# Optimization experiments

Hardware: AMD Instinct MI355X
Metric: run time of the kernel (lower is better)

Reference implementation:

```python
import jax, jax.numpy as jnp
import numpy as np

B, F, O = 32, 26, 20
IN, G = 2048, 512
REL = 53
EPS = 1e-5  # BatchNorm1d default eps


def setup_inputs() -> dict:
    key = jax.random.key(0)
    ks = jax.random.split(key, 10)
    inp = {
        "region_feats": jax.random.normal(ks[0], (B, F, O, IN), jnp.float32),
        "region_masks": jnp.ones((B, F, O), jnp.float32),
        "rel_feats": jax.random.randint(ks[1], (B, F, O, O), 0, REL, jnp.int64),
        "tem_feats": jax.random.uniform(ks[2], (B, F * O, F * O), jnp.float32),
        # learned params (eval mode: dropout off, BN uses running stats)
        "rel_W": jax.random.normal(ks[3], (G, IN), jnp.float32) * (1.0 / np.sqrt(IN)),
        "rel_b": jnp.zeros((G,), jnp.float32),
        "rel_emb": jax.random.normal(ks[4], (REL, G), jnp.float32) * 0.02,
        "tem_W": jax.random.normal(ks[5], (G, IN), jnp.float32) * (1.0 / np.sqrt(IN)),
        "tem_b": jnp.zeros((G,), jnp.float32),
        "bn_w": jnp.ones((F * O,), jnp.float32),
        "bn_b": jnp.zeros((F * O,), jnp.float32),
        "bn_rm": jnp.zeros((F * O,), jnp.float32),
        "bn_rv": jnp.ones((F * O,), jnp.float32),
    }
    return inp


def reference(region_feats, region_masks, rel_feats, tem_feats,
              rel_W, rel_b, rel_emb, tem_W, tem_b,
              bn_w, bn_b, bn_rm, bn_rv):
    b, f, o, _ = region_feats.shape
    # ---- RELATIONAL FEATURE GRAPH ----
    # [B,F,O,G]
    rel_region = jnp.einsum("bfoi,gi->bfog", region_feats, rel_W) + rel_b
    # embedding lookup: [B,F,O,O,G]
    emb = rel_emb[rel_feats]
    mask = (rel_feats > 0).astype(region_feats.dtype)  # [B,F,O,O]
    msum = jnp.sum(mask, axis=3)                        # [B,F,O]
    # sum_j mask_ij * emb_ij  (masked reduction over neighbor dim)
    emb_sum = jnp.einsum("bfijg,bfij->bfig", emb, mask)
    # sum_j mask_ij * r_i == r_i * msum_i, so (emb_sum + r*msum)/msum
    rel_out = (emb_sum + rel_region * msum[..., None]) / msum[..., None]
    rel_out = rel_out.reshape(b, f * o, -1)
    # ---- TEMPORAL FEATURE GRAPH ----
    tem_region = jnp.einsum("bfoi,gi->bfog", region_feats, tem_W) + tem_b
    tem_region = tem_region.reshape(b, f * o, -1)
    tem_sum = jnp.sum(tem_feats, axis=2)                # [B, F*O]
    tem_out = jnp.matmul(tem_feats, tem_region) / tem_sum[..., None]
    # ---- OUTPUT ----
    out = jnp.concatenate([rel_out, tem_out], axis=-1)  # [B, F*O, 2G]
    out = jnp.tanh(out)
    # BatchNorm1d over channel dim 1 (eval mode, running stats)
    inv = bn_w / jnp.sqrt(bn_rv + EPS)                  # [F*O]
    out = (out - bn_rm[None, :, None]) * inv[None, :, None] + bn_b[None, :, None]
    return out
```

## Files before the change

kernel.cpp:

```cpp
#include <hip/hip_runtime.h>
#include <stdint.h>

#define BB 32
#define FO 520
#define M1 16640
#define KIN 2048
#define KA 2112
#define N1 1024
#define GG 512
#define K2P 576
#define M2 640

typedef unsigned short u16;
typedef short v8s __attribute__((ext_vector_type(8)));
typedef float v4f __attribute__((ext_vector_type(4)));

__device__ __forceinline__ u16 f2bf(float f) {
  union { float f; unsigned u; } v; v.f = f;
  unsigned r = v.u + 0x7fffu + ((v.u >> 16) & 1u);
  return (u16)(r >> 16);
}

__device__ __forceinline__ float fast_tanh(float x) {
  float cx = fminf(fmaxf(x, -15.f), 15.f);
  float e = __expf(2.f * cx);
  return (e - 1.f) / (e + 1.f);
}

__global__ void prep_all_kernel(const float* __restrict__ rf, const int* __restrict__ rel,
                                const float* __restrict__ relW, const float* __restrict__ temW,
                                const float* __restrict__ emb, const float* __restrict__ tem,
                                u16* __restrict__ A1, u16* __restrict__ Wc,
                                u16* __restrict__ A2, float* __restrict__ tsum) {
  const int blk = blockIdx.x;
  const int t = threadIdx.x;
  if (blk < M1 + 1024) {
    const float* src;
    u16* orow;
    if (blk < M1) { src = rf + (size_t)blk * KIN; orow = A1 + (size_t)blk * KA; }
    else {
      const int n = blk - M1;
      src = (n < GG) ? (relW + (size_t)n * KIN) : (temW + (size_t)(n - GG) * KIN);
      orow = Wc + (size_t)n * KA;
    }
    const float4* p = (const float4*)src;
    float4 a = p[2 * t], b = p[2 * t + 1];
    v8s v;
    v[0] = (short)f2bf(a.x); v[1] = (short)f2bf(a.y);
    v[2] = (short)f2bf(a.z); v[3] = (short)f2bf(a.w);
    v[4] = (short)f2bf(b.x); v[5] = (short)f2bf(b.y);
    v[6] = (short)f2bf(b.z); v[7] = (short)f2bf(b.w);
    *(v8s*)(orow + t * 8) = v;
    if (t < 64) {
      float sval = 0.f;
      if (blk < M1) {
        const int* rp = rel + (size_t)blk * 20;
        int cnt = 0, ms = 0;
#pragma unroll
        for (int j = 0; j < 20; ++j) { int ix = rp[j]; cnt += (ix == t + 1); ms += (ix > 0); }
        if (t < 52 && ms > 0) sval = (float)cnt / (float)ms;
      } else {
        const int n = blk - M1;
        if (n < GG && t < 52) sval = emb[(size_t)(t + 1) * GG + n];
      }
      orow[KIN + t] = f2bf(sval);
    }
    return;
  }
  const int w = t >> 6, l = t & 63;
  const int row = (blk - (M1 + 1024)) * 4 + w;
  const int b = row / M2, i = row % M2;
  u16* orow = A2 + (size_t)row * K2P;
  v8s z = {0, 0, 0, 0, 0, 0, 0, 0};
  if (i >= FO) {
    *(v8s*)(orow + l * 8) = z;
    if (l < 8) *(v8s*)(orow + (64 + l) * 8) = z;
    return;
  }
  const float* srow = tem + ((size_t)b * FO + i) * FO;
  float s = 0.f;
  {
    float4 a = *(const float4*)(srow + 8 * l);
    float4 bb = *(const float4*)(srow + 8 * l + 4);
    s += a.x + a.y + a.z + a.w + bb.x + bb.y + bb.z + bb.w;
    v8s v;
    v[0] = (short)f2bf(a.x); v[1] = (short)f2bf(a.y);
    v[2] = (short)f2bf(a.z); v[3] = (short)f2bf(a.w);
    v[4] = (short)f2bf(bb.x); v[5] = (short)f2bf(bb.y);
    v[6] = (short)f2bf(bb.z); v[7] = (short)f2bf(bb.w);
    *(v8s*)(orow + l * 8) = v;
  }
  if (l < 8) {
    if (l == 0) {
      float4 a = *(const float4*)(srow + 512);
      float4 bb = *(const float4*)(srow + 516);
      s += a.x + a.y + a.z + a.w + bb.x + bb.y + bb.z + bb.w;
      v8s v;
      v[0] = (short)f2bf(a.x); v[1] = (short)f2bf(a.y);
      v[2] = (short)f2bf(a.z); v[3] = (short)f2bf(a.w);
      v[4] = (short)f2bf(bb.x); v[5] = (short)f2bf(bb.y);
      v[6] = (short)f2bf(bb.z); v[7] = (short)f2bf(bb.w);
      *(v8s*)(orow + 512) = v;
    } else {
      *(v8s*)(orow + (64 + l) * 8) = z;
    }
  }
#pragma unroll
  for (int off = 32; off > 0; off >>= 1) s += __shfl_down(s, off);
  if (l == 0) tsum[(size_t)b * FO + i] = s;
}

__global__ __launch_bounds__(256) void gemm1_kernel(
    const u16* __restrict__ A, const u16* __restrict__ Wc,
    const float* __restrict__ rel_b, const float* __restrict__ tem_b,
    const float* __restrict__ bn_w, const float* __restrict__ bn_b,
    const float* __restrict__ bn_rm, const float* __restrict__ bn_rv,
    float* __restrict__ out, u16* __restrict__ BT) {
  __shared__ u16 smem[8704];
  u16* As = smem;
  u16* Bs = smem + 4096;
  const int tid = threadIdx.x;
  const int lane = tid & 63;
  const int wv = tid >> 6, wm = wv >> 1, wn = wv & 1;
  const int id = blockIdx.x;
  const int x = id & 7, s = id >> 3;
  int mt, ntile;
  if (s < 128) { mt = x * 16 + (s >> 3); ntile = s & 7; }
  else         { mt = 128 + (s - 128);   ntile = x; }
  const int m0 = mt * 128, n0 = ntile * 128;
  const int quad = lane >> 4, r16 = lane & 15;

  const u16* ga[2]; const u16* gb[2];
  u16* la[2]; u16* lb[2];
#pragma unroll
  for (int i = 0; i < 2; ++i) {
    const int L = i * 256 + tid;
    const int r = L >> 2, sl = L & 3;
    const int c = sl ^ ((r >> 1) & 3);
    ga[i] = A + (size_t)(m0 + r) * KA + c * 8;
    gb[i] = Wc + (size_t)(n0 + r) * KA + c * 8;
    la[i] = &As[(size_t)(i * 256 + wv * 64) * 8];
    lb[i] = &Bs[(size_t)(i * 256 + wv * 64) * 8];
  }

  v4f acc[4][4];
#pragma unroll
  for (int i = 0; i < 4; ++i)
#pragma unroll
    for (int j = 0; j < 4; ++j) { v4f z = {0.f, 0.f, 0.f, 0.f}; acc[i][j] = z; }

  for (int k0 = 0; k0 < KA; k0 += 32) {
    __syncthreads();
#pragma unroll
    for (int i = 0; i < 2; ++i) {
      __builtin_amdgcn_global_load_lds((const __attribute__((address_space(1))) void*)ga[i],
                                       (__attribute__((address_space(3))) void*)la[i], 16, 0, 0);
      __builtin_amdgcn_global_load_lds((const __attribute__((address_space(1))) void*)gb[i],
                                       (__attribute__((address_space(3))) void*)lb[i], 16, 0, 0);
      ga[i] += 32; gb[i] += 32;
    }
    __syncthreads();
    v8s af[4], bf[4];
#pragma unroll
    for (int t4 = 0; t4 < 4; ++t4) {
      const int ra = wm * 64 + t4 * 16 + r16;
      const int rb = wn * 64 + t4 * 16 + r16;
      af[t4] = *(const v8s*)&As[ra * 32 + ((quad ^ ((ra >> 1) & 3)) * 8)];
      bf[t4] = *(const v8s*)&Bs[rb * 32 + ((quad ^ ((rb >> 1) & 3)) * 8)];
    }
#pragma unroll
    for (int mtt = 0; mtt < 4; ++mtt)
#pragma unroll
      for (int ntt = 0; ntt < 4; ++ntt)
        acc[mtt][ntt] = __builtin_amdgcn_mfma_f32_16x16x32_bf16(af[mtt], bf[ntt], acc[mtt][ntt], 0, 0, 0);
  }

  if (n0 < GG) {
#pragma unroll
    for (int mtt = 0; mtt < 4; ++mtt) {
      const int mb = m0 + wm * 64 + mtt * 16 + quad * 4;
      const int bb = mb / FO;
      const int fo0 = mb - bb * FO;
      float inv[4], rm[4], bofs[4];
#pragma unroll
      for (int r = 0; r < 4; ++r) {
        const int fo = fo0 + r;
        inv[r] = bn_w[fo] * rsqrtf(bn_rv[fo] + 1e-5f);
        rm[r] = bn_rm[fo]; bofs[r] = bn_b[fo];
      }
#pragma unroll
      for (int ntt = 0; ntt < 4; ++ntt) {
        const int n = n0 + wn * 64 + ntt * 16 + r16;
        const float rbn = rel_b[n];
#pragma unroll
        for (int r = 0; r < 4; ++r) {
          float val = (fast_tanh(acc[mtt][ntt][r] + rbn) - rm[r]) * inv[r] + bofs[r];
          __builtin_nontemporal_store(val, out + (size_t)(mb + r) * N1 + n);
        }
      }
    }
  } else {
    __syncthreads();
#pragma unroll
    for (int p = 0; p < 2; ++p) {
      if (p) __syncthreads();
      if (wn == p) {
#pragma unroll
        for (int mtt = 0; mtt < 4; ++mtt) {
          const int il = wm * 64 + mtt * 16 + quad * 4;
#pragma unroll
          for (int ntt = 0; ntt < 4; ++ntt) {
            const int gl = ntt * 16 + r16;
            const float tb = tem_b[(n0 - GG) + p * 64 + gl];
            ushort4 w;
            w.x = f2bf(acc[mtt][ntt][0] + tb);
            w.y = f2bf(acc[mtt][ntt][1] + tb);
            w.z = f2bf(acc[mtt][ntt][2] + tb);
            w.w = f2bf(acc[mtt][ntt][3] + tb);
            *(ushort4*)&smem[gl * 136 + il] = w;
          }
        }
      }
      __syncthreads();
#pragma unroll
      for (int pass = 0; pass < 4; ++pass) {
        const int gl = pass * 16 + (tid >> 4);
        const int ch = tid & 15;
        const int m = m0 + ch * 8;
        const int b1 = m / FO;
        const int i1 = m - b1 * FO;
        v8s val = *(const v8s*)&smem[gl * 136 + ch * 8];
        const int g = (n0 - GG) + p * 64 + gl;
        *(v8s*)(BT + ((size_t)(b1 * GG + g)) * K2P + i1) = val;
      }
    }
  }
}

__global__ __launch_bounds__(256) void gemm2_kernel(
    const u16* __restrict__ A2, const u16* __restrict__ BT,
    const float* __restrict__ tsum,
    const float* __restrict__ bn_w, const float* __restrict__ bn_b,
    const float* __restrict__ bn_rm, const float* __restrict__ bn_rv,
    float* __restrict__ out) {
  __shared__ u16 smem[2 * 64 * 64];
  u16* As = smem;
  u16* Bs = smem + 4096;
  const int tid = threadIdx.x;
  const int lane = tid & 63;
  const int wv = tid >> 6, wm = wv >> 1, wn = wv & 1;
  const int m0 = blockIdx.x * 64;
  const int n0 = blockIdx.y * 64;
  const int b = blockIdx.z;
  const u16* Ab = A2 + (size_t)b * M2 * K2P;
  const u16* Bb = BT + (size_t)b * GG * K2P;
  const int quad = lane >> 4, r16 = lane & 15;

  const u16* gp[4]; u16* lp[4];
#pragma unroll
  for (int i = 0; i < 4; ++i) {
    const int L = i * 256 + tid;
    const int tile = L >> 9;
    const int idx = L & 511;
    const int r = idx >> 3, sl = idx & 7;
    const int c = sl ^ (r & 7);
    gp[i] = (tile ? (Bb + (size_t)(n0 + r) * K2P) : (Ab + (size_t)(m0 + r) * K2P)) + c * 8;
    lp[i] = (tile ? Bs : As) + (size_t)((i & 1) * 256 + wv * 64) * 8;
  }

  v4f acc[2][2];
#pragma unroll
  for (int i = 0; i < 2; ++i)
#pragma unroll
    for (int j = 0; j < 2; ++j) { v4f z = {0.f, 0.f, 0.f, 0.f}; acc[i][j] = z; }

  for (int k0 = 0; k0 < K2P; k0 += 64) {
    __syncthreads();
#pragma unroll
    for (int i = 0; i < 4; ++i) {
      __builtin_amdgcn_global_load_lds((const __attribute__((address_space(1))) void*)gp[i],
                                       (__attribute__((address_space(3))) void*)lp[i], 16, 0, 0);
      gp[i] += 64;
    }
    __syncthreads();
#pragma unroll
    for (int ks = 0; ks < 2; ++ks) {
      v8s af[2], bf[2];
#pragma unroll
      for (int t4 = 0; t4 < 2; ++t4) {
        const int ra = wm * 32 + t4 * 16 + r16;
        const int rb = wn * 32 + t4 * 16 + r16;
        af[t4] = *(const v8s*)&As[ra * 64 + (((ks * 4 + quad) ^ (ra & 7)) * 8)];
        bf[t4] = *(const v8s*)&Bs[rb * 64 + (((ks * 4 + quad) ^ (rb & 7)) * 8)];
      }
#pragma unroll
      for (int mtt = 0; mtt < 2; ++mtt)
#pragma unroll
        for (int ntt = 0; ntt < 2; ++ntt)
          acc[mtt][ntt] = __builtin_amdgcn_mfma_f32_16x16x32_bf16(af[mtt], bf[ntt], acc[mtt][ntt], 0, 0, 0);
    }
  }

#pragma unroll
  for (int mtt = 0; mtt < 2; ++mtt) {
    const int ibase = m0 + wm * 32 + mtt * 16 + quad * 4;
    float ts[4], inv[4], rm[4], bofs[4];
#pragma unroll
    for (int r = 0; r < 4; ++r) {
      const int i = ibase + r;
      if (i < FO) {
        ts[r] = 1.f / tsum[(size_t)b * FO + i];
        inv[r] = bn_w[i] * rsqrtf(bn_rv[i] + 1e-5f);
        rm[r] = bn_rm[i]; bofs[r] = bn_b[i];
      }
    }
#pragma unroll
    for (int ntt = 0; ntt < 2; ++ntt) {
      const int g = n0 + wn * 32 + ntt * 16 + r16;
#pragma unroll
      for (int r = 0; r < 4; ++r) {
        const int i = ibase + r;
        if (i < FO) {
          float val = (fast_tanh(acc[mtt][ntt][r] * ts[r]) - rm[r]) * inv[r] + bofs[r];
          __builtin_nontemporal_store(val, out + ((size_t)(b * FO + i)) * N1 + GG + g);
        }
      }
    }
  }
}

extern "C" void kernel_launch(void* const* d_in, const int* in_sizes, int n_in,
                              void* d_out, int out_size, void* d_ws, size_t ws_size,
                              hipStream_t stream) {
  const float* region_feats = (const float*)d_in[0];
  const int* rel_feats = (const int*)d_in[2];
  const float* tem_feats = (const float*)d_in[3];
  const float* rel_W = (const float*)d_in[4];
  const float* rel_b = (const float*)d_in[5];
  const float* rel_emb = (const float*)d_in[6];
  const float* tem_W = (const float*)d_in[7];
  const float* tem_b = (const float*)d_in[8];
  const float* bn_w = (const float*)d_in[9];
  const float* bn_b = (const float*)d_in[10];
  const float* bn_rm = (const float*)d_in[11];
  const float* bn_rv = (const float*)d_in[12];
  float* out = (float*)d_out;

  char* base = (char*)d_ws;
  u16* A1 = (u16*)base;
  u16* Wc = (u16*)(base + 70287360);
  u16* A2 = (u16*)(base + 74612736);
  u16* BT = (u16*)(base + 98205696);
  float* tsum = (float*)(base + 117080064);

  prep_all_kernel<<<M1 + 1024 + 5120, 256, 0, stream>>>(
      region_feats, rel_feats, rel_W, tem_W, rel_emb, tem_feats, A1, Wc, A2, tsum);
  gemm1_kernel<<<1040, 256, 0, stream>>>(A1, Wc, rel_b, tem_b,
                                         bn_w, bn_b, bn_rm, bn_rv, out, BT);
  gemm2_kernel<<<dim3(10, 8, 32), 256, 0, stream>>>(A2, BT, tsum,
                                                    bn_w, bn_b, bn_rm, bn_rv, out);
}
```

Measured before the change: 438.2 us.

## Double-buffer LDS tiles in both GEMM kernels to overlap loads with MFMA

Both GEMM kernels now use two LDS stages. The next K-slice is issued with global_load_lds into the alternate buffer while MFMAs run on the current one, which cuts one barrier per iteration and hides global-load latency behind compute. LDS use grows to 32KB per block, which may lower occupancy. Correctness depends on the single trailing __syncthreads also waiting for the async LDS loads (vmcnt) to finish before the buffers swap.

```diff
diff --git a/kernel.cpp b/kernel.cpp
--- a/kernel.cpp
+++ b/kernel.cpp
@@ -116,9 +116,7 @@
     const float* __restrict__ bn_w, const float* __restrict__ bn_b,
     const float* __restrict__ bn_rm, const float* __restrict__ bn_rv,
     float* __restrict__ out, u16* __restrict__ BT) {
-  __shared__ u16 smem[8704];
-  u16* As = smem;
-  u16* Bs = smem + 4096;
+  __shared__ u16 smem[16384];
   const int tid = threadIdx.x;
   const int lane = tid & 63;
   const int wv = tid >> 6, wm = wv >> 1, wn = wv & 1;
@@ -131,7 +129,7 @@
   const int quad = lane >> 4, r16 = lane & 15;
 
   const u16* ga[2]; const u16* gb[2];
-  u16* la[2]; u16* lb[2];
+  int lofA[2], lofB[2];
 #pragma unroll
   for (int i = 0; i < 2; ++i) {
     const int L = i * 256 + tid;
@@ -139,8 +137,8 @@
     const int c = sl ^ ((r >> 1) & 3);
     ga[i] = A + (size_t)(m0 + r) * KA + c * 8;
     gb[i] = Wc + (size_t)(n0 + r) * KA + c * 8;
-    la[i] = &As[(size_t)(i * 256 + wv * 64) * 8];
-    lb[i] = &Bs[(size_t)(i * 256 + wv * 64) * 8];
+    lofA[i] = (i * 256 + wv * 64) * 8;
+    lofB[i] = 4096 + (i * 256 + wv * 64) * 8;
   }
 
   v4f acc[4][4];
@@ -149,17 +147,31 @@
 #pragma unroll
     for (int j = 0; j < 4; ++j) { v4f z = {0.f, 0.f, 0.f, 0.f}; acc[i][j] = z; }
 
+#pragma unroll
+  for (int i = 0; i < 2; ++i) {
+    __builtin_amdgcn_global_load_lds((const __attribute__((address_space(1))) void*)ga[i],
+                                     (__attribute__((address_space(3))) void*)(smem + lofA[i]), 16, 0, 0);
+    __builtin_amdgcn_global_load_lds((const __attribute__((address_space(1))) void*)gb[i],
+                                     (__attribute__((address_space(3))) void*)(smem + lofB[i]), 16, 0, 0);
+    ga[i] += 32; gb[i] += 32;
+  }
+  __syncthreads();
+
+  int cur = 0;
   for (int k0 = 0; k0 < KA; k0 += 32) {
-    __syncthreads();
-#pragma unroll
-    for (int i = 0; i < 2; ++i) {
-      __builtin_amdgcn_global_load_lds((const __attribute__((address_space(1))) void*)ga[i],
-                                       (__attribute__((address_space(3))) void*)la[i], 16, 0, 0);
-      __builtin_amdgcn_global_load_lds((const __attribute__((address_space(1))) void*)gb[i],
-                                       (__attribute__((address_space(3))) void*)lb[i], 16, 0, 0);
-      ga[i] += 32; gb[i] += 32;
-    }
-    __syncthreads();
+    if (k0 + 32 < KA) {
+      u16* dst = smem + (cur ^ 1) * 8192;
+#pragma unroll
+      for (int i = 0; i < 2; ++i) {
+        __builtin_amdgcn_global_load_lds((const __attribute__((address_space(1))) void*)ga[i],
+                                         (__attribute__((address_space(3))) void*)(dst + lofA[i]), 16, 0, 0);
+        __builtin_amdgcn_global_load_lds((const __attribute__((address_space(1))) void*)gb[i],
+                                         (__attribute__((address_space(3))) void*)(dst + lofB[i]), 16, 0, 0);
+        ga[i] += 32; gb[i] += 32;
+      }
+    }
+    const u16* As = smem + cur * 8192;
+    const u16* Bs = As + 4096;
     v8s af[4], bf[4];
 #pragma unroll
     for (int t4 = 0; t4 < 4; ++t4) {
@@ -173,6 +185,8 @@
 #pragma unroll
       for (int ntt = 0; ntt < 4; ++ntt)
         acc[mtt][ntt] = __builtin_amdgcn_mfma_f32_16x16x32_bf16(af[mtt], bf[ntt], acc[mtt][ntt], 0, 0, 0);
+    __syncthreads();
+    cur ^= 1;
   }
 
   if (n0 < GG) {
@@ -243,9 +257,7 @@
     const float* __restrict__ bn_w, const float* __restrict__ bn_b,
     const float* __restrict__ bn_rm, const float* __restrict__ bn_rv,
     float* __restrict__ out) {
-  __shared__ u16 smem[2 * 64 * 64];
-  u16* As = smem;
-  u16* Bs = smem + 4096;
+  __shared__ u16 smem[16384];
   const int tid = threadIdx.x;
   const int lane = tid & 63;
   const int wv = tid >> 6, wm = wv >> 1, wn = wv & 1;
@@ -256,7 +268,7 @@
   const u16* Bb = BT + (size_t)b * GG * K2P;
   const int quad = lane >> 4, r16 = lane & 15;
 
-  const u16* gp[4]; u16* lp[4];
+  const u16* gp[4]; int lof[4];
 #pragma unroll
   for (int i = 0; i < 4; ++i) {
     const int L = i * 256 + tid;
@@ -265,7 +277,7 @@
     const int r = idx >> 3, sl = idx & 7;
     const int c = sl ^ (r & 7);
     gp[i] = (tile ? (Bb + (size_t)(n0 + r) * K2P) : (Ab + (size_t)(m0 + r) * K2P)) + c * 8;
-    lp[i] = (tile ? Bs : As) + (size_t)((i & 1) * 256 + wv * 64) * 8;
+    lof[i] = (tile ? 4096 : 0) + ((i & 1) * 256 + wv * 64) * 8;
   }
 
   v4f acc[2][2];
@@ -274,15 +286,27 @@
 #pragma unroll
     for (int j = 0; j < 2; ++j) { v4f z = {0.f, 0.f, 0.f, 0.f}; acc[i][j] = z; }
 
+#pragma unroll
+  for (int i = 0; i < 4; ++i) {
+    __builtin_amdgcn_global_load_lds((const __attribute__((address_space(1))) void*)gp[i],
+                                     (__attribute__((address_space(3))) void*)(smem + lof[i]), 16, 0, 0);
+    gp[i] += 64;
+  }
+  __syncthreads();
+
+  int cur = 0;
   for (int k0 = 0; k0 < K2P; k0 += 64) {
-    __syncthreads();
-#pragma unroll
-    for (int i = 0; i < 4; ++i) {
-      __builtin_amdgcn_global_load_lds((const __attribute__((address_space(1))) void*)gp[i],
-                                       (__attribute__((address_space(3))) void*)lp[i], 16, 0, 0);
-      gp[i] += 64;
-    }
-    __syncthreads();
+    if (k0 + 64 < K2P) {
+      u16* dst = smem + (cur ^ 1) * 8192;
+#pragma unroll
+      for (int i = 0; i < 4; ++i) {
+        __builtin_amdgcn_global_load_lds((const __attribute__((address_space(1))) void*)gp[i],
+                                         (__attribute__((address_space(3))) void*)(dst + lof[i]), 16, 0, 0);
+        gp[i] += 64;
+      }
+    }
+    const u16* As = smem + cur * 8192;
+    const u16* Bs = As + 4096;
 #pragma unroll
     for (int ks = 0; ks < 2; ++ks) {
       v8s af[2], bf[2];
@@ -299,6 +323,8 @@
         for (int ntt = 0; ntt < 2; ++ntt)
           acc[mtt][ntt] = __builtin_amdgcn_mfma_f32_16x16x32_bf16(af[mtt], bf[ntt], acc[mtt][ntt], 0, 0, 0);
     }
+    __syncthreads();
+    cur ^= 1;
   }
 
 #pragma unroll
```

Result: no change. 431.0 us (-1.6%).

## Triple-buffer LDS pipeline in both GEMMs and enlarge gemm2 tiles

Applied to the files above, without the earlier changes.

Both GEMM kernels replace the single-buffered load-then-compute loop with a three-stage LDS ring. Global-to-LDS loads for K-step t+2 are issued while step t is computed, synchronised with explicit vmcnt waits and s_barrier. The aim is to hide global memory latency behind MFMA work instead of stalling on two __syncthreads per K-step. gemm2 also moves from 64x64 to 128x128 tiles with a 4x4 MFMA fragment per wave, which cuts the block count and increases operand reuse. The cost is more LDS per block (48 KB), which lowers occupancy, and hand-written waitcnt sequencing that must match the number of loads in flight exactly.

```diff
diff --git a/kernel.cpp b/kernel.cpp
--- a/kernel.cpp
+++ b/kernel.cpp
@@ -110,15 +110,57 @@
   if (l == 0) tsum[(size_t)b * FO + i] = s;
 }
 
+
+#define STAGE4(DST)                                                                              \
+  do {                                                                                           \
+    u16* dst_ = smem + (DST);                                                                    \
+    __builtin_amdgcn_global_load_lds((const __attribute__((address_space(1))) void*)ga0,         \
+        (__attribute__((address_space(3))) void*)(dst_ + lofA0), 16, 0, 0);                      \
+    __builtin_amdgcn_global_load_lds((const __attribute__((address_space(1))) void*)gb0,         \
+        (__attribute__((address_space(3))) void*)(dst_ + lofB0), 16, 0, 0);                      \
+    __builtin_amdgcn_global_load_lds((const __attribute__((address_space(1))) void*)ga1,         \
+        (__attribute__((address_space(3))) void*)(dst_ + lofA1), 16, 0, 0);                      \
+    __builtin_amdgcn_global_load_lds((const __attribute__((address_space(1))) void*)gb1,         \
+        (__attribute__((address_space(3))) void*)(dst_ + lofB1), 16, 0, 0);                      \
+    ga0 += 32; gb0 += 32; ga1 += 32; gb1 += 32;                                                  \
+  } while (0)
+
+#define COMPUTE16(CB)                                                                            \
+  do {                                                                                           \
+    const u16* As_ = smem + (CB) * 8192;                                                         \
+    const u16* Bs_ = As_ + 4096;                                                                 \
+    v8s af[4], bf[4];                                                                            \
+    _Pragma("unroll") for (int t4 = 0; t4 < 4; ++t4) {                                           \
+      const int ra = wm * 64 + t4 * 16 + r16;                                                    \
+      const int rb = wn * 64 + t4 * 16 + r16;                                                    \
+      af[t4] = *(const v8s*)&As_[ra * 32 + ((quad ^ ((ra >> 1) & 3)) * 8)];                      \
+      bf[t4] = *(const v8s*)&Bs_[rb * 32 + ((quad ^ ((rb >> 1) & 3)) * 8)];                      \
+    }                                                                                            \
+    _Pragma("unroll") for (int mtt = 0; mtt < 4; ++mtt)                                          \
+      _Pragma("unroll") for (int ntt = 0; ntt < 4; ++ntt)                                        \
+        acc[mtt][ntt] =                                                                          \
+            __builtin_amdgcn_mfma_f32_16x16x32_bf16(af[mtt], bf[ntt], acc[mtt][ntt], 0, 0, 0);   \
+  } while (0)
+
+#define PIPE_TAIL(CB0, CB1)                                                                      \
+  do {                                                                                           \
+    asm volatile("s_waitcnt vmcnt(4)" ::: "memory");                                             \
+    __builtin_amdgcn_s_barrier();                                                                \
+    COMPUTE16(CB0);                                                                              \
+    asm volatile("s_waitcnt lgkmcnt(0)" ::: "memory");                                           \
+    __builtin_amdgcn_s_barrier();                                                                \
+    asm volatile("s_waitcnt vmcnt(0)" ::: "memory");                                             \
+    __builtin_amdgcn_s_barrier();                                                                \
+    COMPUTE16(CB1);                                                                              \
+  } while (0)
+
 __global__ __launch_bounds__(256) void gemm1_kernel(
     const u16* __restrict__ A, const u16* __restrict__ Wc,
     const float* __restrict__ rel_b, const float* __restrict__ tem_b,
     const float* __restrict__ bn_w, const float* __restrict__ bn_b,
     const float* __restrict__ bn_rm, const float* __restrict__ bn_rv,
     float* __restrict__ out, u16* __restrict__ BT) {
-  __shared__ u16 smem[8704];
-  u16* As = smem;
-  u16* Bs = smem + 4096;
+  __shared__ u16 smem[24576];
   const int tid = threadIdx.x;
   const int lane = tid & 63;
   const int wv = tid >> 6, wm = wv >> 1, wn = wv & 1;
@@ -130,18 +172,20 @@
   const int m0 = mt * 128, n0 = ntile * 128;
   const int quad = lane >> 4, r16 = lane & 15;
 
-  const u16* ga[2]; const u16* gb[2];
-  u16* la[2]; u16* lb[2];
-#pragma unroll
-  for (int i = 0; i < 2; ++i) {
-    const int L = i * 256 + tid;
-    const int r = L >> 2, sl = L & 3;
-    const int c = sl ^ ((r >> 1) & 3);
-    ga[i] = A + (size_t)(m0 + r) * KA + c * 8;
-    gb[i] = Wc + (size_t)(n0 + r) * KA + c * 8;
-    la[i] = &As[(size_t)(i * 256 + wv * 64) * 8];
-    lb[i] = &Bs[(size_t)(i * 256 + wv * 64) * 8];
-  }
+  const u16 *ga0, *ga1, *gb0, *gb1;
+  {
+    const int r0 = tid >> 2, sl0 = tid & 3;
+    const int c0 = sl0 ^ ((r0 >> 1) & 3);
+    ga0 = A + (size_t)(m0 + r0) * KA + c0 * 8;
+    gb0 = Wc + (size_t)(n0 + r0) * KA + c0 * 8;
+    const int L1 = 256 + tid;
+    const int r1 = L1 >> 2, sl1 = L1 & 3;
+    const int c1 = sl1 ^ ((r1 >> 1) & 3);
+    ga1 = A + (size_t)(m0 + r1) * KA + c1 * 8;
+    gb1 = Wc + (size_t)(n0 + r1) * KA + c1 * 8;
+  }
+  const int lofA0 = wv * 512, lofA1 = 2048 + wv * 512;
+  const int lofB0 = 4096 + wv * 512, lofB1 = 6144 + wv * 512;
 
   v4f acc[4][4];
 #pragma unroll
@@ -149,31 +193,21 @@
 #pragma unroll
     for (int j = 0; j < 4; ++j) { v4f z = {0.f, 0.f, 0.f, 0.f}; acc[i][j] = z; }
 
-  for (int k0 = 0; k0 < KA; k0 += 32) {
-    __syncthreads();
-#pragma unroll
-    for (int i = 0; i < 2; ++i) {
-      __builtin_amdgcn_global_load_lds((const __attribute__((address_space(1))) void*)ga[i],
-                                       (__attribute__((address_space(3))) void*)la[i], 16, 0, 0);
-      __builtin_amdgcn_global_load_lds((const __attribute__((address_space(1))) void*)gb[i],
-                                       (__attribute__((address_space(3))) void*)lb[i], 16, 0, 0);
-      ga[i] += 32; gb[i] += 32;
-    }
-    __syncthreads();
-    v8s af[4], bf[4];
-#pragma unroll
-    for (int t4 = 0; t4 < 4; ++t4) {
-      const int ra = wm * 64 + t4 * 16 + r16;
-      const int rb = wn * 64 + t4 * 16 + r16;
-      af[t4] = *(const v8s*)&As[ra * 32 + ((quad ^ ((ra >> 1) & 3)) * 8)];
-      bf[t4] = *(const v8s*)&Bs[rb * 32 + ((quad ^ ((rb >> 1) & 3)) * 8)];
-    }
-#pragma unroll
-    for (int mtt = 0; mtt < 4; ++mtt)
-#pragma unroll
-      for (int ntt = 0; ntt < 4; ++ntt)
-        acc[mtt][ntt] = __builtin_amdgcn_mfma_f32_16x16x32_bf16(af[mtt], bf[ntt], acc[mtt][ntt], 0, 0, 0);
-  }
+  STAGE4(0);
+  STAGE4(8192);
+
+  int cb = 0, nb = 2;
+  for (int t = 0; t < 64; ++t) {
+    STAGE4(nb * 8192);
+    asm volatile("s_waitcnt vmcnt(8)" ::: "memory");
+    __builtin_amdgcn_s_barrier();
+    COMPUTE16(cb);
+    asm volatile("s_waitcnt lgkmcnt(0)" ::: "memory");
+    __builtin_amdgcn_s_barrier();
+    cb = (cb == 2) ? 0 : cb + 1;
+    nb = (nb == 2) ? 0 : nb + 1;
+  }
+  PIPE_TAIL(cb, (cb == 2) ? 0 : cb + 1);
 
   if (n0 < GG) {
 #pragma unroll
@@ -243,87 +277,73 @@
     const float* __restrict__ bn_w, const float* __restrict__ bn_b,
     const float* __restrict__ bn_rm, const float* __restrict__ bn_rv,
     float* __restrict__ out) {
-  __shared__ u16 smem[2 * 64 * 64];
-  u16* As = smem;
-  u16* Bs = smem + 4096;
+  __shared__ u16 smem[24576];
   const int tid = threadIdx.x;
   const int lane = tid & 63;
   const int wv = tid >> 6, wm = wv >> 1, wn = wv & 1;
-  const int m0 = blockIdx.x * 64;
-  const int n0 = blockIdx.y * 64;
+  const int m0 = blockIdx.x * 128;
+  const int n0 = blockIdx.y * 128;
   const int b = blockIdx.z;
   const u16* Ab = A2 + (size_t)b * M2 * K2P;
   const u16* Bb = BT + (size_t)b * GG * K2P;
   const int quad = lane >> 4, r16 = lane & 15;
 
-  const u16* gp[4]; u16* lp[4];
-#pragma unroll
-  for (int i = 0; i < 4; ++i) {
-    const int L = i * 256 + tid;
-    const int tile = L >> 9;
-    const int idx = L & 511;
-    const int r = idx >> 3, sl = idx & 7;
-    const int c = sl ^ (r & 7);
-    gp[i] = (tile ? (Bb + (size_t)(n0 + r) * K2P) : (Ab + (size_t)(m0 + r) * K2P)) + c * 8;
-    lp[i] = (tile ? Bs : As) + (size_t)((i & 1) * 256 + wv * 64) * 8;
-  }
-
-  v4f acc[2][2];
-#pragma unroll
-  for (int i = 0; i < 2; ++i)
-#pragma unroll
-    for (int j = 0; j < 2; ++j) { v4f z = {0.f, 0.f, 0.f, 0.f}; acc[i][j] = z; }
-
-  for (int k0 = 0; k0 < K2P; k0 += 64) {
-    __syncthreads();
-#pragma unroll
-    for (int i = 0; i < 4; ++i) {
-      __builtin_amdgcn_global_load_lds((const __attribute__((address_space(1))) void*)gp[i],
-                                       (__attribute__((address_space(3))) void*)lp[i], 16, 0, 0);
-      gp[i] += 64;
-    }
-    __syncthreads();
-#pragma unroll
-    for (int ks = 0; ks < 2; ++ks) {
-      v8s af[2], bf[2];
-#pragma unroll
-      for (int t4 = 0; t4 < 2; ++t4) {
-        const int ra = wm * 32 + t4 * 16 + r16;
-        const int rb = wn * 32 + t4 * 16 + r16;
-        af[t4] = *(const v8s*)&As[ra * 64 + (((ks * 4 + quad) ^ (ra & 7)) * 8)];
-        bf[t4] = *(const v8s*)&Bs[rb * 64 + (((ks * 4 + quad) ^ (rb & 7)) * 8)];
-      }
-#pragma unroll
-      for (int mtt = 0; mtt < 2; ++mtt)
-#pragma unroll
-        for (int ntt = 0; ntt < 2; ++ntt)
-          acc[mtt][ntt] = __builtin_amdgcn_mfma_f32_16x16x32_bf16(af[mtt], bf[ntt], acc[mtt][ntt], 0, 0, 0);
-    }
-  }
-
-#pragma unroll
-  for (int mtt = 0; mtt < 2; ++mtt) {
-    const int ibase = m0 + wm * 32 + mtt * 16 + quad * 4;
+  const u16 *ga0, *ga1, *gb0, *gb1;
+  {
+    const int r0 = tid >> 2, sl0 = tid & 3;
+    const int c0 = sl0 ^ ((r0 >> 1) & 3);
+    ga0 = Ab + (size_t)(m0 + r0) * K2P + c0 * 8;
+    gb0 = Bb + (size_t)(n0 + r0) * K2P + c0 * 8;
+    const int L1 = 256 + tid;
+    const int r1 = L1 >> 2, sl1 = L1 & 3;
+    const int c1 = sl1 ^ ((r1 >> 1) & 3);
+    ga1 = Ab + (size_t)(m0 + r1) * K2P + c1 * 8;
+    gb1 = Bb + (size_t)(n0 + r1) * K2P + c1 * 8;
+  }
+  const int lofA0 = wv * 512, lofA1 = 2048 + wv * 512;
+  const int lofB0 = 4096 + wv * 512, lofB1 = 6144 + wv * 512;
+
+  v4f acc[4][4];
+#pragma unroll
+  for (int i = 0; i < 4; ++i)
+#pragma unroll
+    for (int j = 0; j < 4; ++j) { v4f z = {0.f, 0.f, 0.f, 0.f}; acc[i][j] = z; }
+
+  STAGE4(0);
+  STAGE4(8192);
+
+  int cb = 0, nb = 2;
+  for (int t = 0; t < 16; ++t) {
+    STAGE4(nb * 8192);
+    asm volatile("s_waitcnt vmcnt(8)" ::: "memory");
+    __builtin_amdgcn_s_barrier();
+    COMPUTE16(cb);
+    asm volatile("s_waitcnt lgkmcnt(0)" ::: "memory");
+    __builtin_amdgcn_s_barrier();
+    cb = (cb == 2) ? 0 : cb + 1;
+    nb = (nb == 2) ? 0 : nb + 1;
+  }
+  PIPE_TAIL(cb, (cb == 2) ? 0 : cb + 1);
+
+#pragma unroll
+  for (int mtt = 0; mtt < 4; ++mtt) {
+    const int ibase = m0 + wm * 64 + mtt * 16 + quad * 4;
+    if (ibase >= FO) continue;
     float ts[4], inv[4], rm[4], bofs[4];
 #pragma unroll
     for (int r = 0; r < 4; ++r) {
       const int i = ibase + r;
-      if (i < FO) {
-        ts[r] = 1.f / tsum[(size_t)b * FO + i];
-        inv[r] = bn_w[i] * rsqrtf(bn_rv[i] + 1e-5f);
-        rm[r] = bn_rm[i]; bofs[r] = bn_b[i];
-      }
-    }
-#pragma unroll
-    for (int ntt = 0; ntt < 2; ++ntt) {
-      const int g = n0 + wn * 32 + ntt * 16 + r16;
+      ts[r] = 1.f / tsum[(size_t)b * FO + i];
+      inv[r] = bn_w[i] * rsqrtf(bn_rv[i] + 1e-5f);
+      rm[r] = bn_rm[i]; bofs[r] = bn_b[i];
+    }
+#pragma unroll
+    for (int ntt = 0; ntt < 4; ++ntt) {
+      const int g = n0 + wn * 64 + ntt * 16 + r16;
 #pragma unroll
       for (int r = 0; r < 4; ++r) {
-        const int i = ibase + r;
-        if (i < FO) {
-          float val = (fast_tanh(acc[mtt][ntt][r] * ts[r]) - rm[r]) * inv[r] + bofs[r];
-          __builtin_nontemporal_store(val, out + ((size_t)(b * FO + i)) * N1 + GG + g);
-        }
+        float val = (fast_tanh(acc[mtt][ntt][r] * ts[r]) - rm[r]) * inv[r] + bofs[r];
+        __builtin_nontemporal_store(val, out + ((size_t)(b * FO + (ibase + r))) * N1 + GG + g);
       }
     }
   }
@@ -357,6 +377,6 @@
       region_feats, rel_feats, rel_W, tem_W, rel_emb, tem_feats, A1, Wc, A2, tsum);
   gemm1_kernel<<<1040, 256, 0, stream>>>(A1, Wc, rel_b, tem_b,
                                          bn_w, bn_b, bn_rm, bn_rv, out, BT);
-  gemm2_kernel<<<dim3(10, 8, 32), 256, 0, stream>>>(A2, BT, tsum,
-                                                    bn_w, bn_b, bn_rm, bn_rv, out);
-}
+  gemm2_kernel<<<dim3(5, 4, 32), 256, 0, stream>>>(A2, BT, tsum,
+                                                   bn_w, bn_b, bn_rm, bn_rv, out);
+}
```

Result: faster. 406.6 us (-7.2%).
